# Performance work log

Hardware: AMD Instinct MI355X
Metric: run time of the kernel (lower is better)

Reference implementation:

```python
import jax, jax.numpy as jnp
import numpy as np

N = 262144
C = 256
G = 4096  # number of segments (upper bound on group ids)


def setup_inputs() -> dict:
    key = jax.random.key(0)
    ks = jax.random.split(key, 8)
    s = 1.0 / np.sqrt(C)
    x = jax.random.normal(ks[0], (1, N, C), dtype=jnp.float32)
    ix = jax.random.randint(ks[1], (N,), 0, G, dtype=jnp.int64)
    Wf = jax.random.uniform(ks[2], (C, C), jnp.float32, -s, s)
    bf = jax.random.uniform(ks[3], (C,), jnp.float32, -s, s)
    Wg = jax.random.uniform(ks[4], (C, C), jnp.float32, -s, s)
    bg = jax.random.uniform(ks[5], (C,), jnp.float32, -s, s)
    Wh = jax.random.uniform(ks[6], (C, C), jnp.float32, -s, s)
    bh = jax.random.uniform(ks[7], (C,), jnp.float32, -s, s)
    return {"x": x, "Wf": Wf, "bf": bf, "Wg": Wg, "bg": bg, "Wh": Wh, "bh": bh, "ix": ix}


def reference(x, Wf, bf, Wg, bg, Wh, bh, ix):
    # x: [1, N, C]; only batch 0 is used (matches torch module)
    x0 = x[0]                                    # [N, C]
    fx = x0 @ Wf.T + bf                          # [N, C]
    gx = jnp.clip(x0 @ Wg.T + bg, -50.0, 50.0)   # [N, C]
    exp_gx = jnp.exp(gx)                         # [N, C]
    # Segment softmax: sorting + cumsum group relabel in the torch code is
    # mathematically just a per-group normalized weighted sum keyed by ix.
    seg = ix.astype(jnp.int32)
    denom = jax.ops.segment_sum(exp_gx, seg, num_segments=G)   # [G, C]
    w = exp_gx / denom[seg]                                    # [N, C]
    y = jax.ops.segment_sum(fx * w, seg, num_segments=G)       # [G, C]
    y = y @ Wh.T + bh                                          # [G, C]
    out = y[seg]                                               # [N, C]
    return out[None]                                           # [1, N, C]
```

## Files before the change

kernel.cpp:

```cpp
#include <hip/hip_runtime.h>
#include <stdint.h>
#include <stddef.h>

#define N_ROWS 262144
#define CCH    256
#define NGRP   4096

typedef short bf16x8 __attribute__((ext_vector_type(8)));
typedef short bf16x4 __attribute__((ext_vector_type(4)));
typedef float f32x4  __attribute__((ext_vector_type(4)));
typedef float f32x16 __attribute__((ext_vector_type(16)));

static __device__ __forceinline__ short f2bf(float f){
  union { float f; unsigned u; } v; v.f = f;
  unsigned u = v.u;
  unsigned r = (u + 0x7FFFu + ((u >> 16) & 1u)) >> 16;
  return (short)r;
}

typedef __attribute__((address_space(1))) const unsigned int GU32;
typedef __attribute__((address_space(3))) unsigned int LU32;
static __device__ __forceinline__ void gload_lds16(const void* g, void* l){
  __builtin_amdgcn_global_load_lds((GU32*)g, (LU32*)l, 16, 0, 0);
}


__global__ __launch_bounds__(256) void k_init(
    const float* __restrict__ Wf, const float* __restrict__ Wg,
    const float* __restrict__ Wh,
    short* __restrict__ wfb, short* __restrict__ wgb, float* __restrict__ wht,
    const int* __restrict__ ix, int* __restrict__ counts)
{
  int b = blockIdx.x;
  if (b < 256){
    int e = b * 256 + threadIdx.x;
    wfb[e] = f2bf(Wf[e]);
    wgb[e] = f2bf(Wg[e]);
    int k = e >> 8, j = e & 255;
    wht[e] = Wh[j * 256 + k];
  } else {
    int i = (b - 256) * 256 + threadIdx.x;
    atomicAdd(&counts[ix[i]], 1);
    i += 131072;
    atomicAdd(&counts[ix[i]], 1);
  }
}

__global__ __launch_bounds__(1024) void k_scan(const int* __restrict__ counts,
    int* __restrict__ cursor, int* __restrict__ ofs){
  __shared__ int sums[1024];
  int t = threadIdx.x;
  int base = t * 4;
  int c0 = counts[base], c1 = counts[base+1], c2 = counts[base+2], c3 = counts[base+3];
  sums[t] = c0 + c1 + c2 + c3;
  __syncthreads();
  for (int off = 1; off < 1024; off <<= 1){
    int v = (t >= off) ? sums[t - off] : 0;
    __syncthreads();
    sums[t] += v;
    __syncthreads();
  }
  int prev = (t == 0) ? 0 : sums[t - 1];
  int o0 = prev, o1 = prev + c0, o2 = prev + c0 + c1, o3 = prev + c0 + c1 + c2;
  cursor[base] = o0; cursor[base+1] = o1; cursor[base+2] = o2; cursor[base+3] = o3;
  ofs[base]    = o0; ofs[base+1]    = o1; ofs[base+2]    = o2; ofs[base+3]    = o3;
}

__global__ __launch_bounds__(256) void k_slot(
    const int* __restrict__ ix, int* __restrict__ cursor, int2* __restrict__ po)
{
  int i = blockIdx.x * 256 + threadIdx.x;
  int g = ix[i];
  int p = atomicAdd(&cursor[g], 1);
  po[p] = make_int2(g, i);
}

__global__ __launch_bounds__(256) void k_gather_cast(
    const int2* __restrict__ po, const float* __restrict__ x,
    short* __restrict__ xb)
{
  __shared__ int i_s[128];

  const int tid  = threadIdx.x;
  const int wave = tid >> 6;
  const int lane = tid & 63;
  const int hl   = lane & 31;
  const int sel  = lane >> 5;

  const int base = blockIdx.x * 128;
  if (tid < 128) i_s[tid] = po[base + tid].y;
  __syncthreads();

  const int ks = hl >> 1, half = hl & 1;
  for (int pass = wave; pass < 64; pass += 8){
    int slotA = pass * 2 + sel;
    int slotB = (pass + 4) * 2 + sel;
    int srcA = i_s[slotA], dstA = base + slotA;
    int srcB = i_s[slotB], dstB = base + slotB;
    const float* xpA = x + (size_t)srcA * 256 + hl * 8;
    const float* xpB = x + (size_t)srcB * 256 + hl * 8;
    f32x4 a0 = *(const f32x4*)(xpA);
    f32x4 a1 = *(const f32x4*)(xpA + 4);
    f32x4 b0 = *(const f32x4*)(xpB);
    f32x4 b1 = *(const f32x4*)(xpB + 4);
    bf16x8 ba, bb;
    #pragma unroll
    for (int j = 0; j < 4; ++j){
      ba[j] = f2bf(a0[j]); ba[4+j] = f2bf(a1[j]);
      bb[j] = f2bf(b0[j]); bb[4+j] = f2bf(b1[j]);
    }
    int tA = dstA >> 5, rA = dstA & 31;
    int tB = dstB >> 5, rB = dstB & 31;
    *(bf16x8*)(xb + ((size_t)(tA * 16 + ks) * 512 + rA * 16 + half * 8)) = ba;
    *(bf16x8*)(xb + ((size_t)(tB * 16 + ks) * 512 + rB * 16 + half * 8)) = bb;
  }
}

__global__ __launch_bounds__(256) void k_gemm(
    const short* __restrict__ xb,
    const short* __restrict__ wfb, const short* __restrict__ wgb,
    const float* __restrict__ bfp, const float* __restrict__ bgp,
    const int2* __restrict__ po,
    float* __restrict__ numer, float* __restrict__ denom)
{
  __shared__ short bst[32][512];

  const int tid  = threadIdx.x;
  const int wave = tid >> 6;
  const int lane = tid & 63;
  const int l31  = lane & 31;
  const int hi   = lane >> 5;

  const int p     = blockIdx.x;
  const int xcd   = p & 7;
  const int ixd   = p >> 3;
  const int cg    = ixd & 7;
  const int bslot = xcd * 32 + (ixd >> 3);
  const int j0    = cg * 32;

  #pragma unroll
  for (int q = 0; q < 8; ++q){
    int f = wave * 8 + q;
    int mat = f >> 4, ks = f & 15;
    const short* wsrc = mat ? wgb : wfb;
    const short* src = wsrc + (size_t)(j0 + l31) * 256 + ks * 16 + hi * 8;
    gload_lds16(src, &bst[f][0]);
  }
  __syncthreads();

  bf16x8 Bf[16], Bg[16];
  #pragma unroll
  for (int f = 0; f < 16; ++f){
    Bf[f] = *(const bf16x8*)&bst[f][lane * 8];
    Bg[f] = *(const bf16x8*)&bst[16 + f][lane * 8];
  }

  const float bfv = bfp[j0 + l31];
  const float bgv = bgp[j0 + l31];

#define KSTEP(A, KS) do { \
    accF = __builtin_amdgcn_mfma_f32_32x32x16_bf16((A), Bf[KS], accF, 0, 0, 0); \
    accG = __builtin_amdgcn_mfma_f32_32x32x16_bf16((A), Bg[KS], accG, 0, 0, 0); \
  } while (0)

  const int aoff = l31 * 16 + hi * 8;

  #pragma unroll 1
  for (int tile = bslot; tile < N_ROWS / 128; tile += 256){
    const int tgrp = tile * 4 + wave;
    const int gidv = po[tgrp * 32 + l31].x;
    const short* xr = xb + (size_t)tgrp * 8192 + aoff;

    f32x16 accF, accG;
    #pragma unroll
    for (int r = 0; r < 16; ++r){ accF[r] = 0.f; accG[r] = 0.f; }

    bf16x8 a0 = *(const bf16x8*)(xr + 0 * 512);
    bf16x8 a1 = *(const bf16x8*)(xr + 1 * 512);
    bf16x8 a2 = *(const bf16x8*)(xr + 2 * 512);
    bf16x8 a3 = *(const bf16x8*)(xr + 3 * 512);
    bf16x8 b0 = *(const bf16x8*)(xr + 4 * 512);
    bf16x8 b1 = *(const bf16x8*)(xr + 5 * 512);
    bf16x8 b2 = *(const bf16x8*)(xr + 6 * 512);
    bf16x8 b3 = *(const bf16x8*)(xr + 7 * 512);
    __builtin_amdgcn_s_setprio(1);
    KSTEP(a0, 0); KSTEP(a1, 1); KSTEP(a2, 2); KSTEP(a3, 3);
    a0 = *(const bf16x8*)(xr + 8 * 512);
    a1 = *(const bf16x8*)(xr + 9 * 512);
    a2 = *(const bf16x8*)(xr + 10 * 512);
    a3 = *(const bf16x8*)(xr + 11 * 512);
    KSTEP(b0, 4); KSTEP(b1, 5); KSTEP(b2, 6); KSTEP(b3, 7);
    b0 = *(const bf16x8*)(xr + 12 * 512);
    b1 = *(const bf16x8*)(xr + 13 * 512);
    b2 = *(const bf16x8*)(xr + 14 * 512);
    b3 = *(const bf16x8*)(xr + 15 * 512);
    KSTEP(a0, 8); KSTEP(a1, 9); KSTEP(a2, 10); KSTEP(a3, 11);
    KSTEP(b0, 12); KSTEP(b1, 13); KSTEP(b2, 14); KSTEP(b3, 15);
    __builtin_amdgcn_s_setprio(0);

    #pragma unroll
    for (int r = 0; r < 16; ++r){
      float g = accG[r] + bgv;
      g = fminf(fmaxf(g, -50.f), 50.f);
      float e = __expf(g);
      accF[r] = (accF[r] + bfv) * e;
      accG[r] = e;
    }

    int gprev = __shfl(gidv, (l31 + 31) & 31);
    bool head = (l31 == 0) || (gidv != gprev);
    unsigned long long hb = __ballot(head) & 0xFFFFFFFFull;
    if (hb == 1ull){
      int g = __shfl(gidv, 0);
      float sF = 0.f, sE = 0.f;
      #pragma unroll
      for (int r = 0; r < 16; ++r){ sF += accF[r]; sE += accG[r]; }
      sF += __shfl_xor(sF, 32);
      sE += __shfl_xor(sE, 32);
      if (hi == 0){
        atomicAdd(&numer[(size_t)g * 256 + j0 + l31], sF);
        atomicAdd(&denom[(size_t)g * 256 + j0 + l31], sE);
      }
    } else {
      int start = 0;
      while (start < 32){
        int g = __shfl(gidv, start);
        unsigned long long rest = hb >> (start + 1);
        int end = rest ? (start + 1 + __builtin_ctzll(rest)) : 32;
        float sF = 0.f, sE = 0.f;
        #pragma unroll
        for (int r = 0; r < 16; ++r){
          int row = (r & 3) + 8 * (r >> 2) + 4 * hi;
          bool in = (row >= start) && (row < end);
          sF += in ? accF[r] : 0.f;
          sE += in ? accG[r] : 0.f;
        }
        sF += __shfl_xor(sF, 32);
        sE += __shfl_xor(sE, 32);
        if (hi == 0){
          atomicAdd(&numer[(size_t)g * 256 + j0 + l31], sF);
          atomicAdd(&denom[(size_t)g * 256 + j0 + l31], sE);
        }
        start = end;
      }
    }
  }
#undef KSTEP
}

__global__ __launch_bounds__(256) void k_yh_out(
    const float* __restrict__ numer, const float* __restrict__ denom,
    const float* __restrict__ wht, const float* __restrict__ bh,
    const int* __restrict__ ofs, const int* __restrict__ counts,
    const int2* __restrict__ po, float* __restrict__ out)
{
  __shared__ float ys[8][256];
  int t = threadIdx.x;
  int g0 = blockIdx.x * 8;
  #pragma unroll
  for (int gg = 0; gg < 8; ++gg){
    size_t idx = (size_t)(g0 + gg) * 256 + t;
    float d = denom[idx];
    ys[gg][t] = (d != 0.f) ? (numer[idx] / d) : 0.f;
  }
  __syncthreads();
  float acc[8];
  #pragma unroll
  for (int gg = 0; gg < 8; ++gg) acc[gg] = 0.f;
  for (int k = 0; k < 256; k += 4){
    float w0 = wht[(k+0) * 256 + t];
    float w1 = wht[(k+1) * 256 + t];
    float w2 = wht[(k+2) * 256 + t];
    float w3 = wht[(k+3) * 256 + t];
    #pragma unroll
    for (int gg = 0; gg < 8; ++gg)
      acc[gg] += w0 * ys[gg][k] + w1 * ys[gg][k+1] + w2 * ys[gg][k+2] + w3 * ys[gg][k+3];
  }
  float b = bh[t];
  __syncthreads();
  #pragma unroll
  for (int gg = 0; gg < 8; ++gg) ys[gg][t] = acc[gg] + b;
  __syncthreads();

  const int wave = t >> 6;
  const int lane = t & 63;
  for (int gg = 0; gg < 8; ++gg){
    int g = g0 + gg;
    int o = ofs[g], cnt = counts[g];
    f32x4 v = *(const f32x4*)&ys[gg][lane * 4];
    for (int idx = wave; idx < cnt; idx += 4){
      int dst = po[o + idx].y;
      *(f32x4*)(out + (size_t)dst * 256 + lane * 4) = v;
    }
  }
}

extern "C" void kernel_launch(void* const* d_in, const int* in_sizes, int n_in,
                              void* d_out, int out_size, void* d_ws, size_t ws_size,
                              hipStream_t stream)
{
  const float* x  = (const float*)d_in[0];
  const float* Wf = (const float*)d_in[1];
  const float* bf = (const float*)d_in[2];
  const float* Wg = (const float*)d_in[3];
  const float* bg = (const float*)d_in[4];
  const float* Wh = (const float*)d_in[5];
  const float* bh = (const float*)d_in[6];
  const int*   ix = (const int*)d_in[7];
  float* out = (float*)d_out;

  char* ws = (char*)d_ws;
  float* numer  = (float*)(ws + 0);
  float* denom  = (float*)(ws + 4194304);
  int*   counts = (int*)  (ws + 8388608);
  int*   cursor = (int*)  (ws + 8404992);
  int*   ofs    = (int*)  (ws + 8421376);
  float* wht    = (float*)(ws + 12615680);
  short* wfb    = (short*)(ws + 12877824);
  short* wgb    = (short*)(ws + 13008896);
  int2*  po     = (int2*) (ws + 13139968);

  short* xb = (short*)d_out;

  hipMemsetAsync(ws, 0, 8404992, stream);

  k_init<<<768, 256, 0, stream>>>(Wf, Wg, Wh, wfb, wgb, wht, ix, counts);
  k_scan<<<1, 1024, 0, stream>>>(counts, cursor, ofs);
  k_slot<<<1024, 256, 0, stream>>>(ix, cursor, po);
  k_gather_cast<<<2048, 256, 0, stream>>>(po, x, xb);
  k_gemm<<<2048, 256, 0, stream>>>(xb, wfb, wgb, bf, bg, po, numer, denom);
  k_yh_out<<<512, 256, 0, stream>>>(numer, denom, wht, bh, ofs, counts, po, out);
}
```

Measured before the change: 702.7 us.

## Replace persistent tile loop in gemm kernel with one tile per block

The segmented GEMM kernel no longer loops over eight row tiles per block. It launches 16384 blocks that each handle a single 128-row tile. All sixteen A fragments are loaded up front, overlapping the weight LDS fill, and B fragments are read from LDS per k-step instead of being held in 32 registers. This cuts register pressure and exposes more parallelism, at the cost of reloading the weight slice into LDS once per tile rather than once per eight tiles.

```diff
diff --git a/kernel.cpp b/kernel.cpp
--- a/kernel.cpp
+++ b/kernel.cpp
@@ -131,121 +131,92 @@
   const int l31  = lane & 31;
   const int hi   = lane >> 5;
 
-  const int p     = blockIdx.x;
-  const int xcd   = p & 7;
-  const int ixd   = p >> 3;
-  const int cg    = ixd & 7;
-  const int bslot = xcd * 32 + (ixd >> 3);
-  const int j0    = cg * 32;
-
-  #pragma unroll
-  for (int q = 0; q < 8; ++q){
-    int f = wave * 8 + q;
+  const int p   = blockIdx.x;
+  const int xcd = p & 7;
+  const int q   = p >> 3;
+  const int cg  = q & 7;
+  const int rt  = xcd * 256 + (q >> 3);
+  const int j0  = cg * 32;
+
+  #pragma unroll
+  for (int qq = 0; qq < 8; ++qq){
+    int f = wave * 8 + qq;
     int mat = f >> 4, ks = f & 15;
     const short* wsrc = mat ? wgb : wfb;
     const short* src = wsrc + (size_t)(j0 + l31) * 256 + ks * 16 + hi * 8;
     gload_lds16(src, &bst[f][0]);
   }
-  __syncthreads();
-
-  bf16x8 Bf[16], Bg[16];
-  #pragma unroll
-  for (int f = 0; f < 16; ++f){
-    Bf[f] = *(const bf16x8*)&bst[f][lane * 8];
-    Bg[f] = *(const bf16x8*)&bst[16 + f][lane * 8];
-  }
-
+  const int tgrp = rt * 4 + wave;
+  const int gidv = po[tgrp * 32 + l31].x;
+  const short* xr = xb + (size_t)tgrp * 8192 + l31 * 16 + hi * 8;
+  bf16x8 a[16];
+  #pragma unroll
+  for (int ks = 0; ks < 16; ++ks) a[ks] = *(const bf16x8*)(xr + ks * 512);
   const float bfv = bfp[j0 + l31];
   const float bgv = bgp[j0 + l31];
 
-#define KSTEP(A, KS) do { \
-    accF = __builtin_amdgcn_mfma_f32_32x32x16_bf16((A), Bf[KS], accF, 0, 0, 0); \
-    accG = __builtin_amdgcn_mfma_f32_32x32x16_bf16((A), Bg[KS], accG, 0, 0, 0); \
-  } while (0)
-
-  const int aoff = l31 * 16 + hi * 8;
-
-  #pragma unroll 1
-  for (int tile = bslot; tile < N_ROWS / 128; tile += 256){
-    const int tgrp = tile * 4 + wave;
-    const int gidv = po[tgrp * 32 + l31].x;
-    const short* xr = xb + (size_t)tgrp * 8192 + aoff;
-
-    f32x16 accF, accG;
+  __syncthreads();
+
+  f32x16 accF, accG;
+  #pragma unroll
+  for (int r = 0; r < 16; ++r){ accF[r] = 0.f; accG[r] = 0.f; }
+
+  __builtin_amdgcn_s_setprio(1);
+  #pragma unroll
+  for (int ks = 0; ks < 16; ++ks){
+    bf16x8 bF = *(const bf16x8*)&bst[ks][lane * 8];
+    accF = __builtin_amdgcn_mfma_f32_32x32x16_bf16(a[ks], bF, accF, 0, 0, 0);
+    bf16x8 bG = *(const bf16x8*)&bst[16 + ks][lane * 8];
+    accG = __builtin_amdgcn_mfma_f32_32x32x16_bf16(a[ks], bG, accG, 0, 0, 0);
+  }
+  __builtin_amdgcn_s_setprio(0);
+
+  #pragma unroll
+  for (int r = 0; r < 16; ++r){
+    float g = accG[r] + bgv;
+    g = fminf(fmaxf(g, -50.f), 50.f);
+    float e = __expf(g);
+    accF[r] = (accF[r] + bfv) * e;
+    accG[r] = e;
+  }
+
+  int gprev = __shfl(gidv, (l31 + 31) & 31);
+  bool head = (l31 == 0) || (gidv != gprev);
+  unsigned long long hb = __ballot(head) & 0xFFFFFFFFull;
+  if (hb == 1ull){
+    int g = __shfl(gidv, 0);
+    float sF = 0.f, sE = 0.f;
     #pragma unroll
-    for (int r = 0; r < 16; ++r){ accF[r] = 0.f; accG[r] = 0.f; }
-
-    bf16x8 a0 = *(const bf16x8*)(xr + 0 * 512);
-    bf16x8 a1 = *(const bf16x8*)(xr + 1 * 512);
-    bf16x8 a2 = *(const bf16x8*)(xr + 2 * 512);
-    bf16x8 a3 = *(const bf16x8*)(xr + 3 * 512);
-    bf16x8 b0 = *(const bf16x8*)(xr + 4 * 512);
-    bf16x8 b1 = *(const bf16x8*)(xr + 5 * 512);
-    bf16x8 b2 = *(const bf16x8*)(xr + 6 * 512);
-    bf16x8 b3 = *(const bf16x8*)(xr + 7 * 512);
-    __builtin_amdgcn_s_setprio(1);
-    KSTEP(a0, 0); KSTEP(a1, 1); KSTEP(a2, 2); KSTEP(a3, 3);
-    a0 = *(const bf16x8*)(xr + 8 * 512);
-    a1 = *(const bf16x8*)(xr + 9 * 512);
-    a2 = *(const bf16x8*)(xr + 10 * 512);
-    a3 = *(const bf16x8*)(xr + 11 * 512);
-    KSTEP(b0, 4); KSTEP(b1, 5); KSTEP(b2, 6); KSTEP(b3, 7);
-    b0 = *(const bf16x8*)(xr + 12 * 512);
-    b1 = *(const bf16x8*)(xr + 13 * 512);
-    b2 = *(const bf16x8*)(xr + 14 * 512);
-    b3 = *(const bf16x8*)(xr + 15 * 512);
-    KSTEP(a0, 8); KSTEP(a1, 9); KSTEP(a2, 10); KSTEP(a3, 11);
-    KSTEP(b0, 12); KSTEP(b1, 13); KSTEP(b2, 14); KSTEP(b3, 15);
-    __builtin_amdgcn_s_setprio(0);
-
-    #pragma unroll
-    for (int r = 0; r < 16; ++r){
-      float g = accG[r] + bgv;
-      g = fminf(fmaxf(g, -50.f), 50.f);
-      float e = __expf(g);
-      accF[r] = (accF[r] + bfv) * e;
-      accG[r] = e;
+    for (int r = 0; r < 16; ++r){ sF += accF[r]; sE += accG[r]; }
+    sF += __shfl_xor(sF, 32);
+    sE += __shfl_xor(sE, 32);
+    if (hi == 0){
+      atomicAdd(&numer[(size_t)g * 256 + j0 + l31], sF);
+      atomicAdd(&denom[(size_t)g * 256 + j0 + l31], sE);
     }
-
-    int gprev = __shfl(gidv, (l31 + 31) & 31);
-    bool head = (l31 == 0) || (gidv != gprev);
-    unsigned long long hb = __ballot(head) & 0xFFFFFFFFull;
-    if (hb == 1ull){
-      int g = __shfl(gidv, 0);
+  } else {
+    int start = 0;
+    while (start < 32){
+      int g = __shfl(gidv, start);
+      unsigned long long rest = hb >> (start + 1);
+      int end = rest ? (start + 1 + __builtin_ctzll(rest)) : 32;
       float sF = 0.f, sE = 0.f;
       #pragma unroll
-      for (int r = 0; r < 16; ++r){ sF += accF[r]; sE += accG[r]; }
+      for (int r = 0; r < 16; ++r){
+        int row = (r & 3) + 8 * (r >> 2) + 4 * hi;
+        bool in = (row >= start) && (row < end);
+        sF += in ? accF[r] : 0.f;
+        sE += in ? accG[r] : 0.f;
+      }
       sF += __shfl_xor(sF, 32);
       sE += __shfl_xor(sE, 32);
       if (hi == 0){
         atomicAdd(&numer[(size_t)g * 256 + j0 + l31], sF);
         atomicAdd(&denom[(size_t)g * 256 + j0 + l31], sE);
       }
-    } else {
-      int start = 0;
-      while (start < 32){
-        int g = __shfl(gidv, start);
-        unsigned long long rest = hb >> (start + 1);
-        int end = rest ? (start + 1 + __builtin_ctzll(rest)) : 32;
-        float sF = 0.f, sE = 0.f;
-        #pragma unroll
-        for (int r = 0; r < 16; ++r){
-          int row = (r & 3) + 8 * (r >> 2) + 4 * hi;
-          bool in = (row >= start) && (row < end);
-          sF += in ? accF[r] : 0.f;
-          sE += in ? accG[r] : 0.f;
-        }
-        sF += __shfl_xor(sF, 32);
-        sE += __shfl_xor(sE, 32);
-        if (hi == 0){
-          atomicAdd(&numer[(size_t)g * 256 + j0 + l31], sF);
-          atomicAdd(&denom[(size_t)g * 256 + j0 + l31], sE);
-        }
-        start = end;
-      }
+      start = end;
     }
   }
-#undef KSTEP
 }
 
 __global__ __launch_bounds__(256) void k_yh_out(
@@ -328,6 +299,6 @@
   k_scan<<<1, 1024, 0, stream>>>(counts, cursor, ofs);
   k_slot<<<1024, 256, 0, stream>>>(ix, cursor, po);
   k_gather_cast<<<2048, 256, 0, stream>>>(po, x, xb);
-  k_gemm<<<2048, 256, 0, stream>>>(xb, wfb, wgb, bf, bg, po, numer, denom);
+  k_gemm<<<16384, 256, 0, stream>>>(xb, wfb, wgb, bf, bg, po, numer, denom);
   k_yh_out<<<512, 256, 0, stream>>>(numer, denom, wht, bh, ofs, counts, po, out);
 }
```

New measurement: 712.6 us. Within noise of the previous version (+1.4%).
